# Kernel optimization log

Measured on AMD Instinct MI355X. Metric: run time of the kernel, lower is better.

## Reference

```python
import jax, jax.numpy as jnp
import numpy as np

VAT_TOKENS = 57
ACTION_NUM = 56
NUM_HEADS = 16
DIM = 1152
HEAD_DIM = DIM // NUM_HEADS
SCALE = HEAD_DIM ** -0.5
N_GROUPS = 3  # num_non_act = 768 -> 3 groups of 256


def setup_inputs() -> dict:
    key = jax.random.key(0)
    ks = jax.random.split(key, 8)
    B, N, C = 32, VAT_TOKENS + 768, DIM
    w_std = C ** -0.5
    return {
        "x": jax.random.normal(ks[0], (B, N, C), jnp.float32),
        "w_qkv_non": jax.random.normal(ks[1], (3 * C, C), jnp.float32) * w_std,
        "w_q_act": jax.random.normal(ks[2], (C, C), jnp.float32) * w_std,
        "w_kv_act": jax.random.normal(ks[3], (2 * C, C), jnp.float32) * w_std,
        "w_proj_non": jax.random.normal(ks[4], (C, C), jnp.float32) * w_std,
        "b_proj_non": jnp.zeros((C,), jnp.float32),
        "w_proj_act": jax.random.normal(ks[5], (C, C), jnp.float32) * w_std,
        "b_proj_act": jnp.zeros((C,), jnp.float32),
    }


def reference(x, w_qkv_non, w_q_act, w_kv_act, w_proj_non, b_proj_non,
              w_proj_act, b_proj_act):
    B, N, C = x.shape
    H, Dh = NUM_HEADS, HEAD_DIM
    num_non_act = N - VAT_TOKENS
    G = num_non_act // N_GROUPS  # group size (256)

    # ---- non-action stream: windowed (grouped) self-attention ----
    non_act = x[:, VAT_TOKENS:]                                  # (B, 768, C)
    qkv = non_act @ w_qkv_non.T                                  # (B, 768, 3C)
    qkv = qkv.reshape(B, N_GROUPS, G, 3, H, Dh)
    q = qkv[:, :, :, 0]                                          # (B, g, G, H, Dh)
    k = qkv[:, :, :, 1]
    v = qkv[:, :, :, 2]
    attn = jnp.einsum('bgqhd,bgkhd->bghqk', q, k) * SCALE
    attn = jax.nn.softmax(attn, axis=-1)
    x_non = jnp.einsum('bghqk,bgkhd->bgqhd', attn, v)
    x_non = x_non.reshape(B, num_non_act, C)

    # ---- action stream: act queries attend to x[ACTION_NUM:] ----
    act = x[:, :VAT_TOKENS]
    q_act = (act @ w_q_act.T).reshape(B, VAT_TOKENS, H, Dh)
    kv = (x @ w_kv_act.T).reshape(B, N, 2, H, Dh)
    k_act = kv[:, ACTION_NUM:, 0]                                # (B, N-56, H, Dh)
    v_act = kv[:, ACTION_NUM:, 1]
    attn_act = jnp.einsum('bqhd,bkhd->bhqk', q_act, k_act) * SCALE
    attn_act = jax.nn.softmax(attn_act, axis=-1)
    x_act = jnp.einsum('bhqk,bkhd->bqhd', attn_act, v_act)
    x_act = x_act.reshape(B, VAT_TOKENS, C)

    # ---- output projections + concat ----
    x_non = x_non @ w_proj_non.T + b_proj_non
    x_act = x_act @ w_proj_act.T + b_proj_act
    return jnp.concatenate([x_act, x_non], axis=1)
```

## Files before the change

kernel.cpp:

```cpp
#include <hip/hip_runtime.h>

typedef __attribute__((ext_vector_type(8))) __bf16 bf16x8;
typedef __attribute__((ext_vector_type(4))) float f32x4;
typedef __attribute__((ext_vector_type(4))) unsigned short u16x4;
typedef __attribute__((ext_vector_type(8))) unsigned short u16x8;

#define MFMA_BF16 __builtin_amdgcn_mfma_f32_16x16x32_bf16

__device__ __forceinline__ unsigned short f2bf(float f) {
  union { float f; unsigned u; } v; v.f = f;
  unsigned r = v.u + 0x7FFFu + ((v.u >> 16) & 1u);
  return (unsigned short)(r >> 16);
}

__device__ __forceinline__ void gload16(const void* g, void* l) {
  __builtin_amdgcn_global_load_lds(
      (const __attribute__((address_space(1))) unsigned int*)g,
      (__attribute__((address_space(3))) unsigned int*)l, 16, 0, 0);
}

__device__ __forceinline__ void cast8(const float* __restrict__ in,
                                      unsigned short* __restrict__ out, long i) {
  long base = i * 8;
  float4 a = *(const float4*)(in + base);
  float4 b = *(const float4*)(in + base + 4);
  u16x8 o;
  o[0] = f2bf(a.x); o[1] = f2bf(a.y); o[2] = f2bf(a.z); o[3] = f2bf(a.w);
  o[4] = f2bf(b.x); o[5] = f2bf(b.y); o[6] = f2bf(b.z); o[7] = f2bf(b.w);
  *(u16x8*)(out + base) = o;
}

__global__ void __launch_bounds__(256) cast_all(
    const float* __restrict__ x, const float* __restrict__ wqkv,
    const float* __restrict__ wq, const float* __restrict__ wkv,
    const float* __restrict__ wpn, const float* __restrict__ wpa,
    unsigned short* __restrict__ xb, unsigned short* __restrict__ wqkvb,
    unsigned short* __restrict__ wqb, unsigned short* __restrict__ wkvb,
    unsigned short* __restrict__ wpnb, unsigned short* __restrict__ wpab) {
  const long c0 = 3801600, c1 = 4299264, c2 = 4465152, c3 = 4796928,
             c4 = 4962816, c5 = 5128704;
  long i = (long)blockIdx.x * 256 + threadIdx.x;
  if (i >= c5) return;
  if (i < c0)      cast8(x,    xb,    i);
  else if (i < c1) cast8(wqkv, wqkvb, i - c0);
  else if (i < c2) cast8(wq,   wqb,   i - c1);
  else if (i < c3) cast8(wkv,  wkvb,  i - c2);
  else if (i < c4) cast8(wpn,  wpnb,  i - c3);
  else             cast8(wpa,  wpab,  i - c4);
}

template <int REMAP>
__device__ __forceinline__ long remap_row(int m) {
  if (REMAP == 1) { int b = m / 768; return (long)b * 825 + 57 + (m - b * 768); }
  if (REMAP == 2) { int b = m / 57;  return (long)b * 825 + (m - b * 57); }
  if (REMAP == 3) { int b = m / 769; return (long)b * 825 + 56 + (m - b * 769); }
  return m;
}

template <int REMAP, bool PROJ>
__device__ __forceinline__ void gemm_body(unsigned short* L, int orig, int gx, int nwg,
                                          const unsigned short* __restrict__ A,
                                          const unsigned short* __restrict__ Bw,
                                          void* __restrict__ Cout,
                                          const float* __restrict__ bias,
                                          int M, int N) {
  const int K = 1152;
  unsigned short* Al = L;
  unsigned short* Bl = L + 32768;
  int tid = threadIdx.x;
  int lane = tid & 63;
  int wid = tid >> 6;
  int l15 = lane & 15, hi = lane >> 4;
  int wm = wid >> 2, wn = wid & 3;

  int q8 = nwg >> 3, r8 = nwg & 7;
  int xcd = orig & 7, off = orig >> 3;
  int wgid = (xcd < r8 ? xcd * (q8 + 1) : r8 * (q8 + 1) + (xcd - r8) * q8) + off;
  int bn = wgid % gx, bm = wgid / gx;
  int m0 = bm * 256, n0 = bn * 256;

  int rlo = tid >> 2;
  int cg = ((tid & 3) - (tid >> 3)) & 3;
  int ma0 = m0 + rlo;       if (ma0 > M - 1) ma0 = M - 1;
  int ma1 = m0 + rlo + 128; if (ma1 > M - 1) ma1 = M - 1;
  const unsigned short* aptr0 = A + remap_row<REMAP>(ma0) * K + cg * 8;
  const unsigned short* aptr1 = A + remap_row<REMAP>(ma1) * K + cg * 8;
  int nb0 = n0 + rlo;       if (nb0 > N - 1) nb0 = N - 1;
  int nb1 = n0 + rlo + 128; if (nb1 > N - 1) nb1 = N - 1;
  const unsigned short* bptr0 = Bw + (long)nb0 * K + cg * 8;
  const unsigned short* bptr1 = Bw + (long)nb1 * K + cg * 8;
  unsigned ldst = (unsigned)tid * 8;

  unsigned short* Ad = Al + ldst;
  unsigned short* Bd = Bl + ldst;

  const int cl = (hi + (l15 >> 1)) & 3;
  const unsigned short* arb[4];
  const unsigned short* brb[4];
#pragma unroll
  for (int f = 0; f < 4; ++f) {
    arb[f] = Al + (wm * 128 + f * 16 + l15) * 32 + cl * 8;
    brb[f] = Bl + (wn * 64 + f * 16 + l15) * 32 + cl * 8;
  }

#define STAGE(P)                                                        \
  {                                                                     \
    gload16(aptr0 + (P) * 32, Ad + (((P) & 3) << 13));                  \
    gload16(aptr1 + (P) * 32, Ad + ((((P) & 3) << 13)) + 4096);         \
    gload16(bptr0 + (P) * 32, Bd + (((P) & 3) << 13));                  \
    gload16(bptr1 + (P) * 32, Bd + ((((P) & 3) << 13)) + 4096);         \
  }
#define READ_FA(P, S)                                                   \
  {                                                                     \
    _Pragma("unroll") for (int f = 0; f < 8; ++f)                       \
        fA[S][f] = *(const bf16x8*)(arb[f & 3] + (((P) & 3) << 13) + (f >> 2) * 2048); \
  }
#define READ_FB(P)                                                      \
  {                                                                     \
    _Pragma("unroll") for (int f = 0; f < 4; ++f)                       \
        fB[f] = *(const bf16x8*)(brb[f] + (((P) & 3) << 13));           \
  }

  STAGE(0); STAGE(1); STAGE(2);
  __builtin_amdgcn_sched_barrier(0);
  asm volatile("s_waitcnt vmcnt(4)" ::: "memory");
  __builtin_amdgcn_s_barrier();
  __builtin_amdgcn_sched_barrier(0);

  bf16x8 fA[2][8];
  bf16x8 fB[4];
  READ_FA(0, 0);
  READ_FB(0);
  f32x4 acc[8][4] = {};

#pragma unroll
  for (int p = 0; p < 36; ++p) {
    const int cur = p & 1;
    if (p < 35) READ_FA(p + 1, cur ^ 1);
    __builtin_amdgcn_sched_barrier(0);
    __builtin_amdgcn_s_setprio(1);
#pragma unroll
    for (int fm = 0; fm < 8; ++fm)
#pragma unroll
      for (int fn = 0; fn < 4; ++fn)
        acc[fm][fn] = MFMA_BF16(fA[cur][fm], fB[fn], acc[fm][fn], 0, 0, 0);
    __builtin_amdgcn_s_setprio(0);
    if (p < 35) READ_FB(p + 1);
    if (p <= 32) STAGE(p + 3);
    if (p <= 32)      asm volatile("s_waitcnt vmcnt(4)" ::: "memory");
    else if (p == 33) asm volatile("s_waitcnt vmcnt(0)" ::: "memory");
    if (p < 35) {
      __builtin_amdgcn_sched_barrier(0);
      __builtin_amdgcn_s_barrier();
      __builtin_amdgcn_sched_barrier(0);
    }
  }
#undef STAGE
#undef READ_FA
#undef READ_FB

  if (!PROJ) {
    unsigned short* reg = L + wid * 8192;
#pragma unroll
    for (int a = 0; a < 8; ++a) {
#pragma unroll
      for (int fn = 0; fn < 4; ++fn) {
        int rbase = a * 16 + hi * 4;
#pragma unroll
        for (int r = 0; r < 4; ++r) {
          int row = rbase + r;
          int ch = (fn * 2 + (l15 >> 3)) ^ (row & 7);
          reg[row * 64 + ch * 8 + (l15 & 7)] = f2bf(acc[a][fn][r]);
        }
      }
    }
#pragma unroll
    for (int i = 0; i < 16; ++i) {
      int rr = i * 8 + (lane >> 3);
      int ch = (lane & 7) ^ (rr & 7);
      u16x8 v = *(const u16x8*)(reg + rr * 64 + ch * 8);
      int m = m0 + wm * 128 + rr;
      int n = n0 + wn * 64 + (lane & 7) * 8;
      if (m < M && n < N)
        *(u16x8*)((unsigned short*)Cout + (long)m * N + n) = v;
    }
  } else {
    float* regf = (float*)L + wid * 4096;
    float bv[4];
#pragma unroll
    for (int fn = 0; fn < 4; ++fn) {
      int n = n0 + wn * 64 + fn * 16 + l15;
      bv[fn] = bias[n < N ? n : N - 1];
    }
#pragma unroll
    for (int half = 0; half < 2; ++half) {
#pragma unroll
      for (int a4 = 0; a4 < 4; ++a4) {
#pragma unroll
        for (int fn = 0; fn < 4; ++fn) {
          int rbase = a4 * 16 + hi * 4;
#pragma unroll
          for (int r = 0; r < 4; ++r)
            regf[(rbase + r) * 64 + fn * 16 + l15] = acc[half * 4 + a4][fn][r] + bv[fn];
        }
      }
#pragma unroll
      for (int i = 0; i < 16; ++i) {
        int rr = i * 4 + (lane >> 4);
        int cc = (lane & 15) * 4;
        f32x4 v = *(const f32x4*)(regf + rr * 64 + cc);
        int m = m0 + wm * 128 + half * 64 + rr;
        int n = n0 + wn * 64 + cc;
        if (m < M && n < N)
          *(f32x4*)((float*)Cout + remap_row<REMAP>(m) * N + n) = v;
      }
      if (half == 0) asm volatile("s_waitcnt lgkmcnt(0)" ::: "memory");
    }
  }
}

__global__ void __launch_bounds__(512, 2) gemm_front(
    const unsigned short* __restrict__ xb, const unsigned short* __restrict__ wqkvb,
    const unsigned short* __restrict__ wkvb, const unsigned short* __restrict__ wqb,
    unsigned short* __restrict__ qkvw, unsigned short* __restrict__ kvw,
    unsigned short* __restrict__ qw) {
  __shared__ unsigned short L[65536];
  int bid = blockIdx.x;
  if (bid < 1344)
    gemm_body<1, false>(L, bid, 14, 1344, xb, wqkvb, qkvw, nullptr, 24576, 3456);
  else if (bid < 2217)
    gemm_body<3, false>(L, bid - 1344, 9, 873, xb, wkvb, kvw, nullptr, 24608, 2304);
  else
    gemm_body<2, false>(L, bid - 2217, 5, 40, xb, wqb, qw, nullptr, 1824, 1152);
}

__global__ void __launch_bounds__(512, 2) gemm_proj(
    const unsigned short* __restrict__ attnw, const unsigned short* __restrict__ wpnb,
    const unsigned short* __restrict__ wpab, float* __restrict__ out,
    const float* __restrict__ bpn, const float* __restrict__ bpa) {
  __shared__ unsigned short L[65536];
  int bid = blockIdx.x;
  if (bid < 40)
    gemm_body<2, true>(L, bid, 5, 40, attnw, wpab, out, bpa, 1824, 1152);
  else
    gemm_body<1, true>(L, bid - 40, 5, 480, attnw, wpnb, out, bpn, 24576, 1152);
}

__global__ void __launch_bounds__(256) attn_non(const unsigned short* __restrict__ qkv,
                                                unsigned short* __restrict__ o) {
  int h = blockIdx.x, g = blockIdx.y, b = blockIdx.z;
  __shared__ unsigned short K_s[128 * 104];
  __shared__ unsigned short V_s[80 * 136];
  __shared__ unsigned short P_s[16 * 16 * 40];
  int tid = threadIdx.x, lane = tid & 63, wid = tid >> 6;
  int l15 = lane & 15, hi = lane >> 4;
  const long base = (long)((b * 3 + g) * 256) * 3456;
  const float SC2 = 0.11785113019775793f * 1.4426950408889634f;

  bf16x8 qf[4][3];
#pragma unroll
  for (int qt = 0; qt < 4; qt++)
#pragma unroll
    for (int ds = 0; ds < 3; ds++) {
      int q = wid * 64 + qt * 16 + l15;
      int d = ds * 32 + hi * 8;
      if (d < 72)
        qf[qt][ds] = *(const bf16x8*)(qkv + base + (long)q * 3456 + h * 72 + d);
      else {
        u16x8 z = {0, 0, 0, 0, 0, 0, 0, 0};
        qf[qt][ds] = __builtin_bit_cast(bf16x8, z);
      }
    }

  f32x4 ot[5][4] = {};
  float lsum[4] = {0.f, 0.f, 0.f, 0.f};

  for (int c0 = 0; c0 < 256; c0 += 128) {
    {
      int r = tid >> 1, hf = tid & 1;
      const unsigned short* src = qkv + base + (long)(c0 + r) * 3456 + (16 + h) * 72 + hf * 48;
      unsigned short* dst = &K_s[r * 104 + hf * 48];
#pragma unroll
      for (int j = 0; j < 6; j++) {
        int col = hf * 48 + j * 8;
        u16x8 v = {0, 0, 0, 0, 0, 0, 0, 0};
        if (col < 72) v = *(const u16x8*)(src + j * 8);
        *(u16x8*)(dst + j * 8) = v;
      }
    }
    if (tid < 128) {
      const unsigned short* src = qkv + base + (long)(c0 + tid) * 3456 + (32 + h) * 72;
      u16x8 w[9];
#pragma unroll
      for (int j = 0; j < 9; j++) w[j] = *(const u16x8*)(src + j * 8);
#pragma unroll
      for (int j = 0; j < 9; j++)
#pragma unroll
        for (int e = 0; e < 8; e++) V_s[(j * 8 + e) * 136 + tid] = w[j][e];
    }
    __syncthreads();

#pragma unroll
    for (int k32 = 0; k32 < 4; k32++) {
#pragma unroll
      for (int kt = 0; kt < 2; kt++) {
        bf16x8 kf[3];
#pragma unroll
        for (int ds = 0; ds < 3; ds++)
          kf[ds] = *(const bf16x8*)((const char*)K_s +
                     ((k32 * 32 + kt * 16 + l15) * 104 + ds * 32 + hi * 8) * 2);
#pragma unroll
        for (int qt = 0; qt < 4; qt++) {
          f32x4 st = {};
#pragma unroll
          for (int ds = 0; ds < 3; ds++) st = MFMA_BF16(kf[ds], qf[qt][ds], st, 0, 0, 0);
          u16x4 pw;
#pragma unroll
          for (int r = 0; r < 4; r++) {
            float p = exp2f(st[r] * SC2);
            lsum[qt] += p;
            pw[r] = f2bf(p);
          }
          *(u16x4*)&P_s[((wid * 4 + qt) * 16 + l15) * 40 + kt * 16 + hi * 4] = pw;
        }
      }
      bf16x8 pf[4];
#pragma unroll
      for (int qt = 0; qt < 4; qt++)
        pf[qt] = *(const bf16x8*)&P_s[((wid * 4 + qt) * 16 + l15) * 40 + hi * 8];
#pragma unroll
      for (int dt = 0; dt < 5; dt++) {
        bf16x8 vf = *(const bf16x8*)&V_s[(dt * 16 + l15) * 136 + k32 * 32 + hi * 8];
#pragma unroll
        for (int qt = 0; qt < 4; qt++) ot[dt][qt] = MFMA_BF16(vf, pf[qt], ot[dt][qt], 0, 0, 0);
      }
    }
    __syncthreads();
  }

#pragma unroll
  for (int qt = 0; qt < 4; qt++) {
    float s = lsum[qt];
    s += __shfl_xor(s, 16);
    s += __shfl_xor(s, 32);
    lsum[qt] = 1.0f / s;
  }
#pragma unroll
  for (int dt = 0; dt < 5; dt++)
#pragma unroll
    for (int qt = 0; qt < 4; qt++)
#pragma unroll
      for (int r = 0; r < 4; r++) {
        int d = dt * 16 + hi * 4 + r;
        if (d < 72) {
          long row = (long)b * 825 + 57 + g * 256 + wid * 64 + qt * 16 + l15;
          o[row * 1152 + h * 72 + d] = f2bf(ot[dt][qt][r] * lsum[qt]);
        }
      }
}

__global__ void __launch_bounds__(256) attn_act(const unsigned short* __restrict__ kv,
                                                const unsigned short* __restrict__ qa,
                                                unsigned short* __restrict__ o) {
  int h = blockIdx.x, b = blockIdx.y;
  __shared__ unsigned short K_s[128 * 104];
  __shared__ unsigned short V_s[80 * 136];
  __shared__ unsigned short P_s[4 * 16 * 40];
  int tid = threadIdx.x, lane = tid & 63, wid = tid >> 6;
  int l15 = lane & 15, hi = lane >> 4;
  const float SC2 = 0.11785113019775793f * 1.4426950408889634f;
  const int LIM = 769;

  bf16x8 qf[3];
  {
    int q = wid * 16 + l15; if (q > 56) q = 56;
#pragma unroll
    for (int ds = 0; ds < 3; ds++) {
      int d = ds * 32 + hi * 8;
      if (d < 72)
        qf[ds] = *(const bf16x8*)(qa + (long)(b * 57 + q) * 1152 + h * 72 + d);
      else {
        u16x8 z = {0, 0, 0, 0, 0, 0, 0, 0};
        qf[ds] = __builtin_bit_cast(bf16x8, z);
      }
    }
  }

  f32x4 ot[5] = {};
  float lsum = 0.f;
  const long kbase = (long)b * 769;

  for (int c0 = 0; c0 < LIM; c0 += 128) {
    int valid = LIM - c0; if (valid > 128) valid = 128;
    {
      int r = tid >> 1, hf = tid & 1;
      int rr = r < valid ? r : valid - 1;
      const unsigned short* src = kv + (kbase + c0 + rr) * 2304 + h * 72 + hf * 48;
      unsigned short* dst = &K_s[r * 104 + hf * 48];
#pragma unroll
      for (int j = 0; j < 6; j++) {
        int col = hf * 48 + j * 8;
        u16x8 v = {0, 0, 0, 0, 0, 0, 0, 0};
        if (col < 72) v = *(const u16x8*)(src + j * 8);
        *(u16x8*)(dst + j * 8) = v;
      }
    }
    if (tid < 128) {
      int rr = tid < valid ? tid : valid - 1;
      const unsigned short* src = kv + (kbase + c0 + rr) * 2304 + (16 + h) * 72;
      u16x8 w[9];
#pragma unroll
      for (int j = 0; j < 9; j++) w[j] = *(const u16x8*)(src + j * 8);
#pragma unroll
      for (int j = 0; j < 9; j++)
#pragma unroll
        for (int e = 0; e < 8; e++) V_s[(j * 8 + e) * 136 + tid] = w[j][e];
    }
    __syncthreads();

#pragma unroll
    for (int k32 = 0; k32 < 4; k32++) {
#pragma unroll
      for (int kt = 0; kt < 2; kt++) {
        bf16x8 kf[3];
#pragma unroll
        for (int ds = 0; ds < 3; ds++)
          kf[ds] = *(const bf16x8*)((const char*)K_s +
                     ((k32 * 32 + kt * 16 + l15) * 104 + ds * 32 + hi * 8) * 2);
        f32x4 st = {};
#pragma unroll
        for (int ds = 0; ds < 3; ds++) st = MFMA_BF16(kf[ds], qf[ds], st, 0, 0, 0);
        u16x4 pw;
#pragma unroll
        for (int r = 0; r < 4; r++) {
          int kg = c0 + k32 * 32 + kt * 16 + hi * 4 + r;
          float p = (kg < LIM) ? exp2f(st[r] * SC2) : 0.f;
          lsum += p;
          pw[r] = f2bf(p);
        }
        *(u16x4*)&P_s[(wid * 16 + l15) * 40 + kt * 16 + hi * 4] = pw;
      }
      bf16x8 pf = *(const bf16x8*)&P_s[(wid * 16 + l15) * 40 + hi * 8];
#pragma unroll
      for (int dt = 0; dt < 5; dt++) {
        bf16x8 vf = *(const bf16x8*)&V_s[(dt * 16 + l15) * 136 + k32 * 32 + hi * 8];
        ot[dt] = MFMA_BF16(vf, pf, ot[dt], 0, 0, 0);
      }
    }
    __syncthreads();
  }

  {
    float s = lsum;
    s += __shfl_xor(s, 16);
    s += __shfl_xor(s, 32);
    lsum = 1.0f / s;
  }
  int q = wid * 16 + l15;
#pragma unroll
  for (int dt = 0; dt < 5; dt++)
#pragma unroll
    for (int r = 0; r < 4; r++) {
      int d = dt * 16 + hi * 4 + r;
      if (d < 72 && q < 57)
        o[((long)b * 825 + q) * 1152 + h * 72 + d] = f2bf(ot[dt][r] * lsum);
    }
}

extern "C" void kernel_launch(void* const* d_in, const int* in_sizes, int n_in,
                              void* d_out, int out_size, void* d_ws, size_t ws_size,
                              hipStream_t stream) {
  const float* x     = (const float*)d_in[0];
  const float* w_qkv = (const float*)d_in[1];
  const float* w_q   = (const float*)d_in[2];
  const float* w_kv  = (const float*)d_in[3];
  const float* w_pn  = (const float*)d_in[4];
  const float* b_pn  = (const float*)d_in[5];
  const float* w_pa  = (const float*)d_in[6];
  const float* b_pa  = (const float*)d_in[7];

  char* ws = (char*)d_ws;
  unsigned short* xb    = (unsigned short*)ws; ws += (size_t)26400 * 1152 * 2;
  unsigned short* wqkvb = (unsigned short*)ws; ws += (size_t)3456 * 1152 * 2;
  unsigned short* wqb   = (unsigned short*)ws; ws += (size_t)1152 * 1152 * 2;
  unsigned short* wkvb  = (unsigned short*)ws; ws += (size_t)2304 * 1152 * 2;
  unsigned short* wpnb  = (unsigned short*)ws; ws += (size_t)1152 * 1152 * 2;
  unsigned short* wpab  = (unsigned short*)ws; ws += (size_t)1152 * 1152 * 2;
  unsigned short* qkvw  = (unsigned short*)ws; ws += (size_t)24576 * 3456 * 2;
  unsigned short* kvw   = (unsigned short*)ws; ws += (size_t)24608 * 2304 * 2;
  unsigned short* qw    = (unsigned short*)ws; ws += (size_t)1824 * 1152 * 2;
  unsigned short* attnw = (unsigned short*)ws; ws += (size_t)26400 * 1152 * 2;

  cast_all<<<20034, 256, 0, stream>>>(x, w_qkv, w_q, w_kv, w_pn, w_pa,
                                      xb, wqkvb, wqb, wkvb, wpnb, wpab);

  gemm_front<<<2257, 512, 0, stream>>>(xb, wqkvb, wkvb, wqb, qkvw, kvw, qw);

  attn_non<<<dim3(16, 3, 32), 256, 0, stream>>>(qkvw, attnw);
  attn_act<<<dim3(16, 32), 256, 0, stream>>>(kvw, qw, attnw);

  gemm_proj<<<520, 512, 0, stream>>>(attnw, wpnb, wpab, (float*)d_out, b_pn, b_pa);
}
```

Before: 668.8 us.

## Shrink GEMM tiles to 128x256 with double-buffered LDS and higher occupancy

Halves the M tile of the shared GEMM body from 256 to 128, cuts the LDS pipeline from a 4-stage ring to 2-stage double buffering, and reduces LDS from 128KB to 48KB so launch bounds can ask for 4 workgroups per CU. Grid sizes double, and the epilogues are reorganised into smaller chunks to fit the smaller LDS. The aim is to rely on occupancy rather than deep software prefetch to hide latency. The trade-off is lower arithmetic intensity per tile, and a full vmcnt(0) wait every K step removes the earlier prefetch distance. There is also a risk of register pressure under the 4-wave launch bound.

```diff
diff --git a/kernel.cpp b/kernel.cpp
--- a/kernel.cpp
+++ b/kernel.cpp
@@ -66,7 +66,7 @@
                                           int M, int N) {
   const int K = 1152;
   unsigned short* Al = L;
-  unsigned short* Bl = L + 32768;
+  unsigned short* Bl = L + 8192;
   int tid = threadIdx.x;
   int lane = tid & 63;
   int wid = tid >> 6;
@@ -77,20 +77,17 @@
   int xcd = orig & 7, off = orig >> 3;
   int wgid = (xcd < r8 ? xcd * (q8 + 1) : r8 * (q8 + 1) + (xcd - r8) * q8) + off;
   int bn = wgid % gx, bm = wgid / gx;
-  int m0 = bm * 256, n0 = bn * 256;
+  int m0 = bm * 128, n0 = bn * 256;
 
   int rlo = tid >> 2;
   int cg = ((tid & 3) - (tid >> 3)) & 3;
-  int ma0 = m0 + rlo;       if (ma0 > M - 1) ma0 = M - 1;
-  int ma1 = m0 + rlo + 128; if (ma1 > M - 1) ma1 = M - 1;
-  const unsigned short* aptr0 = A + remap_row<REMAP>(ma0) * K + cg * 8;
-  const unsigned short* aptr1 = A + remap_row<REMAP>(ma1) * K + cg * 8;
+  int ma = m0 + rlo; if (ma > M - 1) ma = M - 1;
+  const unsigned short* aptr = A + remap_row<REMAP>(ma) * K + cg * 8;
   int nb0 = n0 + rlo;       if (nb0 > N - 1) nb0 = N - 1;
   int nb1 = n0 + rlo + 128; if (nb1 > N - 1) nb1 = N - 1;
   const unsigned short* bptr0 = Bw + (long)nb0 * K + cg * 8;
   const unsigned short* bptr1 = Bw + (long)nb1 * K + cg * 8;
   unsigned ldst = (unsigned)tid * 8;
-
   unsigned short* Ad = Al + ldst;
   unsigned short* Bd = Bl + ldst;
 
@@ -99,93 +96,83 @@
   const unsigned short* brb[4];
 #pragma unroll
   for (int f = 0; f < 4; ++f) {
-    arb[f] = Al + (wm * 128 + f * 16 + l15) * 32 + cl * 8;
+    arb[f] = Al + (wm * 64 + f * 16 + l15) * 32 + cl * 8;
     brb[f] = Bl + (wn * 64 + f * 16 + l15) * 32 + cl * 8;
   }
 
-#define STAGE(P)                                                        \
-  {                                                                     \
-    gload16(aptr0 + (P) * 32, Ad + (((P) & 3) << 13));                  \
-    gload16(aptr1 + (P) * 32, Ad + ((((P) & 3) << 13)) + 4096);         \
-    gload16(bptr0 + (P) * 32, Bd + (((P) & 3) << 13));                  \
-    gload16(bptr1 + (P) * 32, Bd + ((((P) & 3) << 13)) + 4096);         \
-  }
-#define READ_FA(P, S)                                                   \
-  {                                                                     \
-    _Pragma("unroll") for (int f = 0; f < 8; ++f)                       \
-        fA[S][f] = *(const bf16x8*)(arb[f & 3] + (((P) & 3) << 13) + (f >> 2) * 2048); \
-  }
-#define READ_FB(P)                                                      \
-  {                                                                     \
-    _Pragma("unroll") for (int f = 0; f < 4; ++f)                       \
-        fB[f] = *(const bf16x8*)(brb[f] + (((P) & 3) << 13));           \
-  }
-
-  STAGE(0); STAGE(1); STAGE(2);
-  __builtin_amdgcn_sched_barrier(0);
-  asm volatile("s_waitcnt vmcnt(4)" ::: "memory");
+#define STAGE(P)                                                  \
+  {                                                               \
+    gload16(aptr + (P) * 32, Ad + (((P) & 1) << 12));             \
+    gload16(bptr0 + (P) * 32, Bd + (((P) & 1) << 13));            \
+    gload16(bptr1 + (P) * 32, Bd + (((P) & 1) << 13) + 4096);     \
+  }
+
+  STAGE(0);
+  asm volatile("s_waitcnt vmcnt(0)" ::: "memory");
   __builtin_amdgcn_s_barrier();
   __builtin_amdgcn_sched_barrier(0);
 
-  bf16x8 fA[2][8];
-  bf16x8 fB[4];
-  READ_FA(0, 0);
-  READ_FB(0);
-  f32x4 acc[8][4] = {};
+  f32x4 acc[4][4] = {};
 
 #pragma unroll
   for (int p = 0; p < 36; ++p) {
-    const int cur = p & 1;
-    if (p < 35) READ_FA(p + 1, cur ^ 1);
-    __builtin_amdgcn_sched_barrier(0);
+    const int sa = (p & 1) << 12;
+    const int sb = (p & 1) << 13;
+    bf16x8 fa[4];
+#pragma unroll
+    for (int f = 0; f < 4; ++f) fa[f] = *(const bf16x8*)(arb[f] + sa);
+    if (p < 35) STAGE(p + 1);
     __builtin_amdgcn_s_setprio(1);
 #pragma unroll
-    for (int fm = 0; fm < 8; ++fm)
-#pragma unroll
-      for (int fn = 0; fn < 4; ++fn)
-        acc[fm][fn] = MFMA_BF16(fA[cur][fm], fB[fn], acc[fm][fn], 0, 0, 0);
+    for (int fn = 0; fn < 4; ++fn) {
+      bf16x8 fb = *(const bf16x8*)(brb[fn] + sb);
+#pragma unroll
+      for (int fm = 0; fm < 4; ++fm)
+        acc[fm][fn] = MFMA_BF16(fa[fm], fb, acc[fm][fn], 0, 0, 0);
+    }
     __builtin_amdgcn_s_setprio(0);
-    if (p < 35) READ_FB(p + 1);
-    if (p <= 32) STAGE(p + 3);
-    if (p <= 32)      asm volatile("s_waitcnt vmcnt(4)" ::: "memory");
-    else if (p == 33) asm volatile("s_waitcnt vmcnt(0)" ::: "memory");
     if (p < 35) {
+      asm volatile("s_waitcnt vmcnt(0)" ::: "memory");
       __builtin_amdgcn_sched_barrier(0);
       __builtin_amdgcn_s_barrier();
       __builtin_amdgcn_sched_barrier(0);
     }
   }
 #undef STAGE
-#undef READ_FA
-#undef READ_FB
+  __syncthreads();
 
   if (!PROJ) {
-    unsigned short* reg = L + wid * 8192;
-#pragma unroll
-    for (int a = 0; a < 8; ++a) {
-#pragma unroll
-      for (int fn = 0; fn < 4; ++fn) {
-        int rbase = a * 16 + hi * 4;
-#pragma unroll
-        for (int r = 0; r < 4; ++r) {
-          int row = rbase + r;
-          int ch = (fn * 2 + (l15 >> 3)) ^ (row & 7);
-          reg[row * 64 + ch * 8 + (l15 & 7)] = f2bf(acc[a][fn][r]);
+    unsigned short* reg = L + wid * 2048;
+#pragma unroll
+    for (int half = 0; half < 2; ++half) {
+#pragma unroll
+      for (int a2 = 0; a2 < 2; ++a2) {
+        int a = half * 2 + a2;
+#pragma unroll
+        for (int fn = 0; fn < 4; ++fn) {
+#pragma unroll
+          for (int r = 0; r < 4; ++r) {
+            int row = a2 * 16 + hi * 4 + r;
+            int ch = (fn * 2 + (l15 >> 3)) ^ (row & 7);
+            reg[row * 64 + ch * 8 + (l15 & 7)] = f2bf(acc[a][fn][r]);
+          }
         }
       }
-    }
-#pragma unroll
-    for (int i = 0; i < 16; ++i) {
-      int rr = i * 8 + (lane >> 3);
-      int ch = (lane & 7) ^ (rr & 7);
-      u16x8 v = *(const u16x8*)(reg + rr * 64 + ch * 8);
-      int m = m0 + wm * 128 + rr;
-      int n = n0 + wn * 64 + (lane & 7) * 8;
-      if (m < M && n < N)
-        *(u16x8*)((unsigned short*)Cout + (long)m * N + n) = v;
+      asm volatile("s_waitcnt lgkmcnt(0)" ::: "memory");
+#pragma unroll
+      for (int i = 0; i < 4; ++i) {
+        int rr = i * 8 + (lane >> 3);
+        int ch = (lane & 7) ^ (rr & 7);
+        u16x8 v = *(const u16x8*)(reg + rr * 64 + ch * 8);
+        int m = m0 + wm * 64 + half * 32 + rr;
+        int n = n0 + wn * 64 + (lane & 7) * 8;
+        if (m < M && n < N)
+          *(u16x8*)((unsigned short*)Cout + (long)m * N + n) = v;
+      }
+      if (half == 0) asm volatile("s_waitcnt lgkmcnt(0)" ::: "memory");
     }
   } else {
-    float* regf = (float*)L + wid * 4096;
+    float* regf = (float*)L + wid * 1024;
     float bv[4];
 #pragma unroll
     for (int fn = 0; fn < 4; ++fn) {
@@ -193,57 +180,53 @@
       bv[fn] = bias[n < N ? n : N - 1];
     }
 #pragma unroll
-    for (int half = 0; half < 2; ++half) {
-#pragma unroll
-      for (int a4 = 0; a4 < 4; ++a4) {
-#pragma unroll
-        for (int fn = 0; fn < 4; ++fn) {
-          int rbase = a4 * 16 + hi * 4;
-#pragma unroll
-          for (int r = 0; r < 4; ++r)
-            regf[(rbase + r) * 64 + fn * 16 + l15] = acc[half * 4 + a4][fn][r] + bv[fn];
-        }
-      }
-#pragma unroll
-      for (int i = 0; i < 16; ++i) {
+    for (int a = 0; a < 4; ++a) {
+#pragma unroll
+      for (int fn = 0; fn < 4; ++fn)
+#pragma unroll
+        for (int r = 0; r < 4; ++r)
+          regf[(hi * 4 + r) * 64 + fn * 16 + l15] = acc[a][fn][r] + bv[fn];
+      asm volatile("s_waitcnt lgkmcnt(0)" ::: "memory");
+#pragma unroll
+      for (int i = 0; i < 4; ++i) {
         int rr = i * 4 + (lane >> 4);
         int cc = (lane & 15) * 4;
         f32x4 v = *(const f32x4*)(regf + rr * 64 + cc);
-        int m = m0 + wm * 128 + half * 64 + rr;
+        int m = m0 + wm * 64 + a * 16 + rr;
         int n = n0 + wn * 64 + cc;
         if (m < M && n < N)
           *(f32x4*)((float*)Cout + remap_row<REMAP>(m) * N + n) = v;
       }
-      if (half == 0) asm volatile("s_waitcnt lgkmcnt(0)" ::: "memory");
-    }
-  }
-}
-
-__global__ void __launch_bounds__(512, 2) gemm_front(
+      if (a < 3) asm volatile("s_waitcnt lgkmcnt(0)" ::: "memory");
+    }
+  }
+}
+
+__global__ void __launch_bounds__(512, 4) gemm_front(
     const unsigned short* __restrict__ xb, const unsigned short* __restrict__ wqkvb,
     const unsigned short* __restrict__ wkvb, const unsigned short* __restrict__ wqb,
     unsigned short* __restrict__ qkvw, unsigned short* __restrict__ kvw,
     unsigned short* __restrict__ qw) {
-  __shared__ unsigned short L[65536];
+  __shared__ unsigned short L[24576];
   int bid = blockIdx.x;
-  if (bid < 1344)
-    gemm_body<1, false>(L, bid, 14, 1344, xb, wqkvb, qkvw, nullptr, 24576, 3456);
-  else if (bid < 2217)
-    gemm_body<3, false>(L, bid - 1344, 9, 873, xb, wkvb, kvw, nullptr, 24608, 2304);
+  if (bid < 2688)
+    gemm_body<1, false>(L, bid, 14, 2688, xb, wqkvb, qkvw, nullptr, 24576, 3456);
+  else if (bid < 4425)
+    gemm_body<3, false>(L, bid - 2688, 9, 1737, xb, wkvb, kvw, nullptr, 24608, 2304);
   else
-    gemm_body<2, false>(L, bid - 2217, 5, 40, xb, wqb, qw, nullptr, 1824, 1152);
-}
-
-__global__ void __launch_bounds__(512, 2) gemm_proj(
+    gemm_body<2, false>(L, bid - 4425, 5, 75, xb, wqb, qw, nullptr, 1824, 1152);
+}
+
+__global__ void __launch_bounds__(512, 4) gemm_proj(
     const unsigned short* __restrict__ attnw, const unsigned short* __restrict__ wpnb,
     const unsigned short* __restrict__ wpab, float* __restrict__ out,
     const float* __restrict__ bpn, const float* __restrict__ bpa) {
-  __shared__ unsigned short L[65536];
+  __shared__ unsigned short L[24576];
   int bid = blockIdx.x;
-  if (bid < 40)
-    gemm_body<2, true>(L, bid, 5, 40, attnw, wpab, out, bpa, 1824, 1152);
+  if (bid < 75)
+    gemm_body<2, true>(L, bid, 5, 75, attnw, wpab, out, bpa, 1824, 1152);
   else
-    gemm_body<1, true>(L, bid - 40, 5, 480, attnw, wpnb, out, bpn, 24576, 1152);
+    gemm_body<1, true>(L, bid - 75, 5, 960, attnw, wpnb, out, bpn, 24576, 1152);
 }
 
 __global__ void __launch_bounds__(256) attn_non(const unsigned short* __restrict__ qkv,
@@ -494,10 +477,10 @@
   cast_all<<<20034, 256, 0, stream>>>(x, w_qkv, w_q, w_kv, w_pn, w_pa,
                                       xb, wqkvb, wqb, wkvb, wpnb, wpab);
 
-  gemm_front<<<2257, 512, 0, stream>>>(xb, wqkvb, wkvb, wqb, qkvw, kvw, qw);
+  gemm_front<<<4500, 512, 0, stream>>>(xb, wqkvb, wkvb, wqb, qkvw, kvw, qw);
 
   attn_non<<<dim3(16, 3, 32), 256, 0, stream>>>(qkvw, attnw);
   attn_act<<<dim3(16, 32), 256, 0, stream>>>(kvw, qw, attnw);
 
-  gemm_proj<<<520, 512, 0, stream>>>(attnw, wpnb, wpab, (float*)d_out, b_pn, b_pa);
-}
+  gemm_proj<<<1035, 512, 0, stream>>>(attnw, wpnb, wpab, (float*)d_out, b_pn, b_pa);
+}
```

After: 672.3 us. Within noise of the previous version (+0.5%).
